# Performance work log

Hardware: AMD Instinct MI355X
Metric: run time of the kernel (lower is better)

## Reference

```python
import jax, jax.numpy as jnp
import numpy as np

C = 256
HEADS = 8
HD = C // HEADS
SCALE = HD ** -0.5


def conv1x1(x, W, b):
    # x: [B,C_in,H,W], W: [C_out,C_in], b: [C_out]
    return jnp.einsum('oc,bchw->bohw', W, x) + b[None, :, None, None]


def setup_inputs() -> dict:
    key = jax.random.key(0)
    ks = jax.random.split(key, 12)
    B, H, Wd = 2, 48, 48
    s = C ** -0.5
    return {
        'x': jax.random.normal(ks[0], (B, C, H, Wd), jnp.float32),
        'uncertainty': jax.random.uniform(ks[1], (B, 1, H, Wd), jnp.float32),
        'Wq': jax.random.normal(ks[2], (C, C), jnp.float32) * s,
        'bq': jnp.zeros((C,), jnp.float32),
        'Wk': jax.random.normal(ks[3], (C, C), jnp.float32) * s,
        'bk': jnp.zeros((C,), jnp.float32),
        'Wv': jax.random.normal(ks[4], (C, C), jnp.float32) * s,
        'bv': jnp.zeros((C,), jnp.float32),
        'Wg': jax.random.normal(ks[5], (C, 1), jnp.float32),
        'bg': jnp.zeros((C,), jnp.float32),
        'Wo': jax.random.normal(ks[6], (C, C), jnp.float32) * s,
        'bo': jnp.zeros((C,), jnp.float32),
    }


def reference(x, uncertainty, Wq, bq, Wk, bk, Wv, bv, Wg, bg, Wo, bo):
    B, _, H, Wd = x.shape
    N = H * Wd
    # uncertainty gate (1x1 conv from 1 channel to C channels)
    uw = conv1x1(uncertainty, Wg, bg)            # [B,C,H,W]
    gated_x = x * (1.0 - uw)
    q = conv1x1(gated_x, Wq, bq).reshape(B, HEADS, HD, N)
    k = conv1x1(gated_x, Wk, bk).reshape(B, HEADS, HD, N)
    v = conv1x1(x, Wv, bv).reshape(B, HEADS, HD, N)
    # scores: [B,h,N,N] (query tokens n, key tokens m)
    scores = jnp.einsum('bhdn,bhdm->bhnm', q, k) * SCALE
    u_flat = uncertainty.reshape(B, 1, 1, N)      # mask over key axis
    scores = scores * (1.0 - u_flat)
    attn = jax.nn.softmax(scores, axis=-1)
    out = jnp.einsum('bhnm,bhdm->bhdn', attn, v)  # [B,h,hd,N]
    out = out.reshape(B, C, H, Wd)
    out = conv1x1(out, Wo, bo)
    return out + x
```

## Files before the change

kernel.cpp:

```cpp
#include <hip/hip_runtime.h>
#include <hip/hip_bf16.h>

typedef float f32x4 __attribute__((ext_vector_type(4)));
typedef __bf16 bf16x8 __attribute__((ext_vector_type(8)));
typedef __bf16 bf16x4 __attribute__((ext_vector_type(4)));
typedef short s16x4 __attribute__((ext_vector_type(4)));

constexpr int C = 256;
constexpr int N = 2304;
constexpr int T = 2 * N;

#if __has_builtin(__builtin_amdgcn_exp2f)
#define EXP2F(x) __builtin_amdgcn_exp2f(x)
#else
#define EXP2F(x) exp2f(x)
#endif

__device__ __forceinline__ bf16x8 load_bf8(const __bf16* p) {
    return *reinterpret_cast<const bf16x8*>(p);
}

__device__ __forceinline__ f32x4 mfma32(bf16x8 a, bf16x8 b, f32x4 c) {
    return __builtin_amdgcn_mfma_f32_16x16x32_bf16(a, b, c, 0, 0, 0);
}

#if __has_builtin(__builtin_amdgcn_mfma_f32_16x16x16bf16_1k)
__device__ __forceinline__ f32x4 mfma16(bf16x4 a, bf16x4 b, f32x4 c) {
    return __builtin_amdgcn_mfma_f32_16x16x16bf16_1k(
        __builtin_bit_cast(s16x4, a), __builtin_bit_cast(s16x4, b), c, 0, 0, 0);
}
#else
__device__ __forceinline__ f32x4 mfma16(bf16x4 a, bf16x4 b, f32x4 c) {
    f32x4 d;
    asm volatile("v_mfma_f32_16x16x16_bf16 %0, %1, %2, %3"
                 : "=v"(d) : "v"(a), "v"(b), "v"(c));
    return d;
}
#endif

__device__ __forceinline__ void gload_lds16(const __bf16* g, __bf16* l) {
    __builtin_amdgcn_global_load_lds(
        (const __attribute__((address_space(1))) void*)g,
        (__attribute__((address_space(3))) void*)l, 16, 0, 0);
}

#define VMCNT2() asm volatile("s_waitcnt vmcnt(2)" ::: "memory")
#define VMCNT0() asm volatile("s_waitcnt vmcnt(0)" ::: "memory")
#define LGKM0()  asm volatile("s_waitcnt lgkmcnt(0)" ::: "memory")

__global__ void wconv_kernel(const float* __restrict__ Wq, const float* __restrict__ Wk,
                             const float* __restrict__ Wv, const float* __restrict__ Wo,
                             __bf16* __restrict__ Wb) {
    const float* srcs[4] = {Wq, Wk, Wv, Wo};
    int m = blockIdx.x >> 6;
    int idx = (blockIdx.x & 63) * 256 + threadIdx.x;
    float4 v = reinterpret_cast<const float4*>(srcs[m])[idx];
    bf16x4 o = { (__bf16)v.x, (__bf16)v.y, (__bf16)v.z, (__bf16)v.w };
    reinterpret_cast<bf16x4*>(Wb + m * 65536)[idx] = o;
}

__global__ void prep_kernel(const float* __restrict__ x, const float* __restrict__ u,
                            const float* __restrict__ Wg, const float* __restrict__ bg,
                            __bf16* __restrict__ xT, __bf16* __restrict__ gxT) {
    __shared__ float tile[64][65];
    int b = blockIdx.z, c0 = blockIdx.y * 64, n0 = blockIdx.x * 64;
    int t = threadIdx.x;
    const float* xp = x + (b * C + c0) * N + n0;
    #pragma unroll
    for (int r = 0; r < 16; ++r) {
        int cl = r * 4 + (t >> 6);
        int nl = t & 63;
        tile[cl][nl] = xp[cl * N + nl];
    }
    __syncthreads();
    int cq = (t & 15) * 4;
    #pragma unroll
    for (int it = 0; it < 4; ++it) {
        int nl = it * 16 + (t >> 4);
        float uv = u[b * N + n0 + nl];
        bf16x4 xo, go;
        #pragma unroll
        for (int j = 0; j < 4; ++j) {
            int c = c0 + cq + j;
            float xv = tile[cq + j][nl];
            float gate = 1.0f - (Wg[c] * uv + bg[c]);
            xo[j] = (__bf16)xv;
            go[j] = (__bf16)(xv * gate);
        }
        int tok = b * N + n0 + nl;
        *reinterpret_cast<bf16x4*>(xT + (long)tok * C + c0 + cq) = xo;
        *reinterpret_cast<bf16x4*>(gxT + (long)tok * C + c0 + cq) = go;
    }
}

__global__ __launch_bounds__(256) void qkv_kernel(const __bf16* __restrict__ Wb,
    const __bf16* __restrict__ xT, const __bf16* __restrict__ gxT,
    const float* __restrict__ bq, const float* __restrict__ bk, const float* __restrict__ bv,
    const float* __restrict__ u,
    __bf16* __restrict__ Q, __bf16* __restrict__ K, __bf16* __restrict__ V) {
    int proj = blockIdx.z;
    int o0 = blockIdx.y * 64;
    int t0 = blockIdx.x * 32;
    int wave = threadIdx.x >> 6, lane = threadIdx.x & 63;
    int g = lane >> 4, r = lane & 15;
    int ow = o0 + wave * 16;
    const __bf16* W = Wb + proj * 65536;
    const __bf16* inp = (proj == 2) ? xT : gxT;
    f32x4 acc[2] = {};
    for (int k = 0; k < 8; ++k) {
        bf16x8 a = load_bf8(W + (ow + r) * C + k * 32 + g * 8);
        #pragma unroll
        for (int tb = 0; tb < 2; ++tb) {
            bf16x8 bfr = load_bf8(inp + (long)(t0 + tb * 16 + r) * C + k * 32 + g * 8);
            acc[tb] = mfma32(a, bfr, acc[tb]);
        }
    }
    const float* bias = (proj == 0) ? bq : (proj == 1) ? bk : bv;
    float bvw[4];
    #pragma unroll
    for (int i = 0; i < 4; ++i) bvw[i] = bias[ow + g * 4 + i];
    int h = ow >> 5, d0 = (ow & 31) + g * 4;
    const float SC = 0.17677669529663687f * 1.4426950408889634f;
    #pragma unroll
    for (int tb = 0; tb < 2; ++tb) {
        int t = t0 + tb * 16 + r;
        int b = t / N, n = t % N;
        if (proj == 2) {
            #pragma unroll
            for (int i = 0; i < 4; ++i)
                V[((long)(b * 8 + h) * 32 + d0 + i) * N + n] = (__bf16)(acc[tb][i] + bvw[i]);
        } else {
            bf16x4 outv;
            if (proj == 1) {
                float scale = SC * (1.0f - u[t]);
                #pragma unroll
                for (int i = 0; i < 4; ++i) outv[i] = (__bf16)((acc[tb][i] + bvw[i]) * scale);
            } else {
                #pragma unroll
                for (int i = 0; i < 4; ++i) outv[i] = (__bf16)(acc[tb][i] + bvw[i]);
            }
            __bf16* dst = (proj == 0) ? Q : K;
            *reinterpret_cast<bf16x4*>(dst + ((long)(b * 8 + h) * N + n) * 32 + d0) = outv;
        }
    }
}

__global__ __launch_bounds__(256) void attn_kernel(const __bf16* __restrict__ Q,
    const __bf16* __restrict__ K, const __bf16* __restrict__ V,
    __bf16* __restrict__ aoT) {
    __shared__ __bf16 sK[2][2048];
    __shared__ __bf16 sV[2][2048];
    int id = blockIdx.x;
    int xcd = id & 7, j = id >> 3;
    int bh = xcd + 8 * (j / 36);
    int qblk = j % 36;
    int wave = threadIdx.x >> 6, lane = threadIdx.x & 63;
    int g = lane >> 4, r = lane & 15;
    int q0w = qblk * 64 + wave * 16;
    const __bf16* Qg = Q + (long)bh * N * 32;
    const __bf16* Kg = K + (long)bh * N * 32;
    const __bf16* Vg = V + (long)bh * 32 * N;
    bf16x8 qf = load_bf8(Qg + (q0w + r) * 32 + g * 8);
    long ksrc = (long)(wave * 64 + lane) * 8;
    int vd = wave * 8 + (lane >> 3);
    long vsrc = (long)vd * N + ((lane & 7) ^ (lane >> 3)) * 8;
    __bf16* sKb = &sK[0][0];
    __bf16* sVb = &sV[0][0];
    int sOff = wave * 512;
    bf16x4 onesv;
    #pragma unroll
    for (int i = 0; i < 4; ++i) onesv[i] = (__bf16)1.0f;
    f32x4 oa0 = {}, oa1 = {}, oal = {};
    gload_lds16(Kg + ksrc, sKb + sOff);
    gload_lds16(Vg + vsrc, sVb + sOff);
    gload_lds16(Kg + 64 * 32 + ksrc, sKb + 2048 + sOff);
    gload_lds16(Vg + vsrc + 64, sVb + 2048 + sOff);
    int vswz = (r & 7) << 3;
    for (int t = 0; t < 36; ++t) {
        if (t < 35) { VMCNT2(); } else { VMCNT0(); }
        __builtin_amdgcn_s_barrier();
        const __bf16* kb = sKb + (t & 1) * 2048;
        const __bf16* vb = sVb + (t & 1) * 2048;
        bf16x8 kc0 = load_bf8(kb + (0 * 16 + r) * 32 + g * 8);
        bf16x8 kc1 = load_bf8(kb + (1 * 16 + r) * 32 + g * 8);
        bf16x8 kc2 = load_bf8(kb + (2 * 16 + r) * 32 + g * 8);
        bf16x8 kc3 = load_bf8(kb + (3 * 16 + r) * 32 + g * 8);
        bf16x4 vf[4][2];
        #pragma unroll
        for (int tt = 0; tt < 4; ++tt)
            #pragma unroll
            for (int dt = 0; dt < 2; ++dt)
                vf[tt][dt] = *reinterpret_cast<const bf16x4*>(
                    vb + (dt * 16 + r) * 64 + ((tt * 16 + g * 4) ^ vswz));
        f32x4 z = {};
        __builtin_amdgcn_s_setprio(1);
        f32x4 s0 = mfma32(kc0, qf, z);
        f32x4 s1 = mfma32(kc1, qf, z);
        f32x4 s2 = mfma32(kc2, qf, z);
        f32x4 s3 = mfma32(kc3, qf, z);
        __builtin_amdgcn_s_setprio(0);
        bf16x4 pa0, pa1, pa2, pa3;
        #pragma unroll
        for (int i = 0; i < 4; ++i) pa0[i] = (__bf16)EXP2F(s0[i]);
        #pragma unroll
        for (int i = 0; i < 4; ++i) pa1[i] = (__bf16)EXP2F(s1[i]);
        #pragma unroll
        for (int i = 0; i < 4; ++i) pa2[i] = (__bf16)EXP2F(s2[i]);
        #pragma unroll
        for (int i = 0; i < 4; ++i) pa3[i] = (__bf16)EXP2F(s3[i]);
        __builtin_amdgcn_s_setprio(1);
        oa0 = mfma16(vf[0][0], pa0, oa0);
        oa1 = mfma16(vf[0][1], pa0, oa1);
        oal = mfma16(onesv,    pa0, oal);
        oa0 = mfma16(vf[1][0], pa1, oa0);
        oa1 = mfma16(vf[1][1], pa1, oa1);
        oal = mfma16(onesv,    pa1, oal);
        oa0 = mfma16(vf[2][0], pa2, oa0);
        oa1 = mfma16(vf[2][1], pa2, oa1);
        oal = mfma16(onesv,    pa2, oal);
        oa0 = mfma16(vf[3][0], pa3, oa0);
        oa1 = mfma16(vf[3][1], pa3, oa1);
        oal = mfma16(onesv,    pa3, oal);
        __builtin_amdgcn_s_setprio(0);
        LGKM0();
        __builtin_amdgcn_s_barrier();
        if (t < 34) {
            long m0n = (long)(t + 2) * 64;
            gload_lds16(Kg + m0n * 32 + ksrc, sKb + (t & 1) * 2048 + sOff);
            gload_lds16(Vg + vsrc + m0n, sVb + (t & 1) * 2048 + sOff);
        }
    }
    float inv = 1.0f / oal[0];
    int b = bh >> 3, h = bh & 7;
    long tok = (long)b * N + q0w + r;
    bf16x4 ov0, ov1;
    #pragma unroll
    for (int i = 0; i < 4; ++i) ov0[i] = (__bf16)(oa0[i] * inv);
    #pragma unroll
    for (int i = 0; i < 4; ++i) ov1[i] = (__bf16)(oa1[i] * inv);
    *reinterpret_cast<bf16x4*>(aoT + tok * C + h * 32 + g * 4) = ov0;
    *reinterpret_cast<bf16x4*>(aoT + tok * C + h * 32 + 16 + g * 4) = ov1;
}

__global__ __launch_bounds__(256) void outp_kernel(const __bf16* __restrict__ Wb,
    const __bf16* __restrict__ aoT, const float* __restrict__ bo,
    const float* __restrict__ x, float* __restrict__ out) {
    int o0 = blockIdx.y * 64;
    int t0 = blockIdx.x * 32;
    int wave = threadIdx.x >> 6, lane = threadIdx.x & 63;
    int g = lane >> 4, r = lane & 15;
    int ow = o0 + wave * 16;
    const __bf16* W = Wb + 3 * 65536;
    f32x4 acc[2] = {};
    for (int k = 0; k < 8; ++k) {
        bf16x8 a = load_bf8(W + (ow + r) * C + k * 32 + g * 8);
        #pragma unroll
        for (int tb = 0; tb < 2; ++tb) {
            bf16x8 bfr = load_bf8(aoT + (long)(t0 + tb * 16 + r) * C + k * 32 + g * 8);
            acc[tb] = mfma32(a, bfr, acc[tb]);
        }
    }
    float bvw[4];
    #pragma unroll
    for (int i = 0; i < 4; ++i) bvw[i] = bo[ow + g * 4 + i];
    #pragma unroll
    for (int tb = 0; tb < 2; ++tb) {
        int t = t0 + tb * 16 + r;
        int b = t / N, n = t % N;
        #pragma unroll
        for (int i = 0; i < 4; ++i) {
            long idx = ((long)b * C + ow + g * 4 + i) * N + n;
            out[idx] = acc[tb][i] + bvw[i] + x[idx];
        }
    }
}

extern "C" void kernel_launch(void* const* d_in, const int* in_sizes, int n_in,
                              void* d_out, int out_size, void* d_ws, size_t ws_size,
                              hipStream_t stream) {
    const float* x  = (const float*)d_in[0];
    const float* u  = (const float*)d_in[1];
    const float* Wq = (const float*)d_in[2];
    const float* bq = (const float*)d_in[3];
    const float* Wk = (const float*)d_in[4];
    const float* bk = (const float*)d_in[5];
    const float* Wv = (const float*)d_in[6];
    const float* bv = (const float*)d_in[7];
    const float* Wg = (const float*)d_in[8];
    const float* bg = (const float*)d_in[9];
    const float* Wo = (const float*)d_in[10];
    const float* bo = (const float*)d_in[11];
    float* out = (float*)d_out;

    char* ws = (char*)d_ws;
    size_t off = 0;
    auto alloc = [&](size_t bytes) {
        char* p = ws + off;
        off += (bytes + 255) & ~(size_t)255;
        return p;
    };
    __bf16* Wb  = (__bf16*)alloc((size_t)4 * 65536 * 2);
    __bf16* xT  = (__bf16*)alloc((size_t)T * C * 2);
    __bf16* gxT = (__bf16*)alloc((size_t)T * C * 2);
    __bf16* Qb  = (__bf16*)alloc((size_t)16 * N * 32 * 2);
    __bf16* Kb  = (__bf16*)alloc((size_t)16 * N * 32 * 2);
    __bf16* Vb  = (__bf16*)alloc((size_t)16 * N * 32 * 2);
    __bf16* aoT = (__bf16*)alloc((size_t)T * C * 2);

    wconv_kernel<<<256, 256, 0, stream>>>(Wq, Wk, Wv, Wo, Wb);
    prep_kernel<<<dim3(36, 4, 2), 256, 0, stream>>>(x, u, Wg, bg, xT, gxT);
    qkv_kernel<<<dim3(144, 4, 3), 256, 0, stream>>>(Wb, xT, gxT, bq, bk, bv, u, Qb, Kb, Vb);
    attn_kernel<<<576, 256, 0, stream>>>(Qb, Kb, Vb, aoT);
    outp_kernel<<<dim3(144, 4), 256, 0, stream>>>(Wb, aoT, bo, x, out);
}
```

Before: 81.15 us.

## Retile prep/outp kernels, swizzle attention LDS staging, use nontemporal QKV stores

Halves the channel tile in prep_kernel and the token tile in outp_kernel so both launch twice as many blocks. Replaces the attention kernel's K/V LDS staging with an XOR-swizzled layout and precomputed per-lane read offsets, to cut LDS bank conflicts. QKV outputs are now written with nontemporal stores. Smaller tiles lower per-block reuse of the W loads in outp, and nontemporal stores may keep Q/K/V out of cache right before the attention kernel reads them.

After: 84.19 us. +3.7%, slower.

```diff
diff --git a/kernel.cpp b/kernel.cpp
--- a/kernel.cpp
+++ b/kernel.cpp
@@ -42,6 +42,15 @@
     __builtin_amdgcn_global_load_lds(
         (const __attribute__((address_space(1))) void*)g,
         (__attribute__((address_space(3))) void*)l, 16, 0, 0);
+}
+
+__device__ __forceinline__ void nt_store4(__bf16* p, bf16x4 v) {
+    __builtin_nontemporal_store(__builtin_bit_cast(long long, v),
+                                reinterpret_cast<long long*>(p));
+}
+__device__ __forceinline__ void nt_store1(__bf16* p, __bf16 v) {
+    __builtin_nontemporal_store(__builtin_bit_cast(short, v),
+                                reinterpret_cast<short*>(p));
 }
 
 #define VMCNT2() asm volatile("s_waitcnt vmcnt(2)" ::: "memory")
@@ -62,21 +71,21 @@
 __global__ void prep_kernel(const float* __restrict__ x, const float* __restrict__ u,
                             const float* __restrict__ Wg, const float* __restrict__ bg,
                             __bf16* __restrict__ xT, __bf16* __restrict__ gxT) {
-    __shared__ float tile[64][65];
-    int b = blockIdx.z, c0 = blockIdx.y * 64, n0 = blockIdx.x * 64;
+    __shared__ float tile[32][65];
+    int b = blockIdx.z, c0 = blockIdx.y * 32, n0 = blockIdx.x * 64;
     int t = threadIdx.x;
     const float* xp = x + (b * C + c0) * N + n0;
     #pragma unroll
-    for (int r = 0; r < 16; ++r) {
+    for (int r = 0; r < 8; ++r) {
         int cl = r * 4 + (t >> 6);
         int nl = t & 63;
         tile[cl][nl] = xp[cl * N + nl];
     }
     __syncthreads();
-    int cq = (t & 15) * 4;
-    #pragma unroll
-    for (int it = 0; it < 4; ++it) {
-        int nl = it * 16 + (t >> 4);
+    int cq = (t & 7) * 4;
+    #pragma unroll
+    for (int it = 0; it < 2; ++it) {
+        int nl = it * 32 + (t >> 3);
         float uv = u[b * N + n0 + nl];
         bf16x4 xo, go;
         #pragma unroll
@@ -128,7 +137,8 @@
         if (proj == 2) {
             #pragma unroll
             for (int i = 0; i < 4; ++i)
-                V[((long)(b * 8 + h) * 32 + d0 + i) * N + n] = (__bf16)(acc[tb][i] + bvw[i]);
+                nt_store1(V + ((long)(b * 8 + h) * 32 + d0 + i) * N + n,
+                          (__bf16)(acc[tb][i] + bvw[i]));
         } else {
             bf16x4 outv;
             if (proj == 1) {
@@ -140,7 +150,7 @@
                 for (int i = 0; i < 4; ++i) outv[i] = (__bf16)(acc[tb][i] + bvw[i]);
             }
             __bf16* dst = (proj == 0) ? Q : K;
-            *reinterpret_cast<bf16x4*>(dst + ((long)(b * 8 + h) * N + n) * 32 + d0) = outv;
+            nt_store4(dst + ((long)(b * 8 + h) * N + n) * 32 + d0, outv);
         }
     }
 }
@@ -154,44 +164,54 @@
     int xcd = id & 7, j = id >> 3;
     int bh = xcd + 8 * (j / 36);
     int qblk = j % 36;
-    int wave = threadIdx.x >> 6, lane = threadIdx.x & 63;
+    int tid = threadIdx.x;
+    int wave = tid >> 6, lane = tid & 63;
     int g = lane >> 4, r = lane & 15;
     int q0w = qblk * 64 + wave * 16;
     const __bf16* Qg = Q + (long)bh * N * 32;
     const __bf16* Kg = K + (long)bh * N * 32;
     const __bf16* Vg = V + (long)bh * 32 * N;
     bf16x8 qf = load_bf8(Qg + (q0w + r) * 32 + g * 8);
-    long ksrc = (long)(wave * 64 + lane) * 8;
-    int vd = wave * 8 + (lane >> 3);
-    long vsrc = (long)vd * N + ((lane & 7) ^ (lane >> 3)) * 8;
-    __bf16* sKb = &sK[0][0];
-    __bf16* sVb = &sV[0][0];
-    int sOff = wave * 512;
+    int l_ = tid ^ ((tid >> 3) & 7);
+    const __bf16* kS = Kg + (l_ >> 2) * 32 + (l_ & 3) * 8;
+    const __bf16* vS = Vg + (long)(l_ >> 3) * N + (l_ & 7) * 8;
+    int so = wave * 512;
+    auto STAGE = [&](long m0, __bf16* kd, __bf16* vd) {
+        gload_lds16(kS + m0 * 32, kd + so);
+        gload_lds16(vS + m0,      vd + so);
+    };
+    int pk[4], pv[4][2];
+    #pragma unroll
+    for (int t = 0; t < 4; ++t) {
+        int ck = (t * 16 + r) * 4 + g;
+        pk[t] = (ck ^ ((ck >> 3) & 7)) * 8;
+        #pragma unroll
+        for (int dt = 0; dt < 2; ++dt) {
+            int cv = (dt * 16 + r) * 8 + t * 2 + (g >> 1);
+            pv[t][dt] = (cv ^ ((cv >> 3) & 7)) * 8 + (g & 1) * 4;
+        }
+    }
     bf16x4 onesv;
     #pragma unroll
     for (int i = 0; i < 4; ++i) onesv[i] = (__bf16)1.0f;
     f32x4 oa0 = {}, oa1 = {}, oal = {};
-    gload_lds16(Kg + ksrc, sKb + sOff);
-    gload_lds16(Vg + vsrc, sVb + sOff);
-    gload_lds16(Kg + 64 * 32 + ksrc, sKb + 2048 + sOff);
-    gload_lds16(Vg + vsrc + 64, sVb + 2048 + sOff);
-    int vswz = (r & 7) << 3;
+    STAGE(0,  &sK[0][0], &sV[0][0]);
+    STAGE(64, &sK[1][0], &sV[1][0]);
     for (int t = 0; t < 36; ++t) {
         if (t < 35) { VMCNT2(); } else { VMCNT0(); }
         __builtin_amdgcn_s_barrier();
-        const __bf16* kb = sKb + (t & 1) * 2048;
-        const __bf16* vb = sVb + (t & 1) * 2048;
-        bf16x8 kc0 = load_bf8(kb + (0 * 16 + r) * 32 + g * 8);
-        bf16x8 kc1 = load_bf8(kb + (1 * 16 + r) * 32 + g * 8);
-        bf16x8 kc2 = load_bf8(kb + (2 * 16 + r) * 32 + g * 8);
-        bf16x8 kc3 = load_bf8(kb + (3 * 16 + r) * 32 + g * 8);
+        const __bf16* kb = &sK[t & 1][0];
+        const __bf16* vb = &sV[t & 1][0];
+        bf16x8 kc0 = load_bf8(kb + pk[0]);
+        bf16x8 kc1 = load_bf8(kb + pk[1]);
+        bf16x8 kc2 = load_bf8(kb + pk[2]);
+        bf16x8 kc3 = load_bf8(kb + pk[3]);
         bf16x4 vf[4][2];
         #pragma unroll
         for (int tt = 0; tt < 4; ++tt)
             #pragma unroll
             for (int dt = 0; dt < 2; ++dt)
-                vf[tt][dt] = *reinterpret_cast<const bf16x4*>(
-                    vb + (dt * 16 + r) * 64 + ((tt * 16 + g * 4) ^ vswz));
+                vf[tt][dt] = *reinterpret_cast<const bf16x4*>(vb + pv[tt][dt]);
         f32x4 z = {};
         __builtin_amdgcn_s_setprio(1);
         f32x4 s0 = mfma32(kc0, qf, z);
@@ -224,11 +244,8 @@
         __builtin_amdgcn_s_setprio(0);
         LGKM0();
         __builtin_amdgcn_s_barrier();
-        if (t < 34) {
-            long m0n = (long)(t + 2) * 64;
-            gload_lds16(Kg + m0n * 32 + ksrc, sKb + (t & 1) * 2048 + sOff);
-            gload_lds16(Vg + vsrc + m0n, sVb + (t & 1) * 2048 + sOff);
-        }
+        if (t < 34)
+            STAGE((long)(t + 2) * 64, &sK[t & 1][0], &sV[t & 1][0]);
     }
     float inv = 1.0f / oal[0];
     int b = bh >> 3, h = bh & 7;
@@ -246,32 +263,26 @@
     const __bf16* __restrict__ aoT, const float* __restrict__ bo,
     const float* __restrict__ x, float* __restrict__ out) {
     int o0 = blockIdx.y * 64;
-    int t0 = blockIdx.x * 32;
+    int t0 = blockIdx.x * 16;
     int wave = threadIdx.x >> 6, lane = threadIdx.x & 63;
     int g = lane >> 4, r = lane & 15;
     int ow = o0 + wave * 16;
     const __bf16* W = Wb + 3 * 65536;
-    f32x4 acc[2] = {};
+    f32x4 acc = {};
     for (int k = 0; k < 8; ++k) {
         bf16x8 a = load_bf8(W + (ow + r) * C + k * 32 + g * 8);
-        #pragma unroll
-        for (int tb = 0; tb < 2; ++tb) {
-            bf16x8 bfr = load_bf8(aoT + (long)(t0 + tb * 16 + r) * C + k * 32 + g * 8);
-            acc[tb] = mfma32(a, bfr, acc[tb]);
-        }
+        bf16x8 bfr = load_bf8(aoT + (long)(t0 + r) * C + k * 32 + g * 8);
+        acc = mfma32(a, bfr, acc);
     }
     float bvw[4];
     #pragma unroll
     for (int i = 0; i < 4; ++i) bvw[i] = bo[ow + g * 4 + i];
-    #pragma unroll
-    for (int tb = 0; tb < 2; ++tb) {
-        int t = t0 + tb * 16 + r;
-        int b = t / N, n = t % N;
-        #pragma unroll
-        for (int i = 0; i < 4; ++i) {
-            long idx = ((long)b * C + ow + g * 4 + i) * N + n;
-            out[idx] = acc[tb][i] + bvw[i] + x[idx];
-        }
+    int t = t0 + r;
+    int b = t / N, n = t % N;
+    #pragma unroll
+    for (int i = 0; i < 4; ++i) {
+        long idx = ((long)b * C + ow + g * 4 + i) * N + n;
+        out[idx] = acc[i] + bvw[i] + x[idx];
     }
 }
 
@@ -308,8 +319,8 @@
     __bf16* aoT = (__bf16*)alloc((size_t)T * C * 2);
 
     wconv_kernel<<<256, 256, 0, stream>>>(Wq, Wk, Wv, Wo, Wb);
-    prep_kernel<<<dim3(36, 4, 2), 256, 0, stream>>>(x, u, Wg, bg, xT, gxT);
+    prep_kernel<<<dim3(36, 8, 2), 256, 0, stream>>>(x, u, Wg, bg, xT, gxT);
     qkv_kernel<<<dim3(144, 4, 3), 256, 0, stream>>>(Wb, xT, gxT, bq, bk, bv, u, Qb, Kb, Vb);
     attn_kernel<<<576, 256, 0, stream>>>(Qb, Kb, Vb, aoT);
-    outp_kernel<<<dim3(144, 4), 256, 0, stream>>>(Wb, aoT, bo, x, out);
-}
+    outp_kernel<<<dim3(288, 4), 256, 0, stream>>>(Wb, aoT, bo, x, out);
+}
```
